# Performance work log

Hardware: AMD Instinct MI355X
Metric: run time of the kernel (lower is better)

The kernel has to match this reference:

```python
import jax, jax.numpy as jnp
import numpy as np

B, T, D, U = 64, 512, 512, 1024


def setup_inputs() -> dict:
    key = jax.random.key(0)
    k1, k2, k3 = jax.random.split(key, 3)
    x = jax.random.normal(k1, (B, T, D), dtype=jnp.float32)
    kernel = jax.random.normal(k2, (D, 4 * U), dtype=jnp.float32) * (1.0 / np.sqrt(D))
    rec_kernel = jax.random.normal(k3, (U, 4 * U), dtype=jnp.float32) * (1.0 / np.sqrt(U))
    return {"x": x, "kernel": kernel, "rec_kernel": rec_kernel}


def reference(x, kernel, rec_kernel):
    """SimpleLSTM forward: returns last hidden state h_T of shape [B, U].
    Gate order along the 4U axis is (i, f, c, o), matching the kernel split.
    No biases; initial h and c are zeros (as in the original call()).
    """
    units = rec_kernel.shape[0]
    # Precompute input contributions for all timesteps in one big GEMM:
    # x_gates[b, t, :] == x[b, t] @ kernel  (same math as 4 per-gate matmuls)
    x_gates = jnp.einsum('btd,dk->tbk', x, kernel)  # [T, B, 4U]

    def step(carry, xt):
        h, c = carry
        z = xt + h @ rec_kernel  # [B, 4U]
        i = jax.nn.sigmoid(z[:, :units])
        f = jax.nn.sigmoid(z[:, units:2 * units])
        g = jnp.tanh(z[:, 2 * units:3 * units])
        o = jax.nn.sigmoid(z[:, 3 * units:])
        c_new = f * c + i * g
        h_new = o * jnp.tanh(c_new)
        return (h_new, c_new), None

    batch = x.shape[0]
    h0 = jnp.zeros((batch, units), dtype=x.dtype)
    c0 = jnp.zeros((batch, units), dtype=x.dtype)
    (h_last, _), _ = jax.lax.scan(step, (h0, c0), x_gates)
    return h_last
```

## Files before the change

### kernel.cpp

```cpp
#include <hip/hip_runtime.h>
#include <stdint.h>

#define WS_XB   0LL
#define WS_H    33554432LL
#define WS_FLAG 33816576LL

typedef unsigned short u16;
typedef unsigned int   u32;
typedef unsigned long long u64;
typedef __attribute__((ext_vector_type(8))) short short8;
typedef __attribute__((ext_vector_type(4))) float f32x4;

__device__ __forceinline__ u16 f2bf(float f) {
  unsigned u = __float_as_uint(f);
  u += 0x7FFFu + ((u >> 16) & 1u);
  return (u16)(u >> 16);
}
__device__ __forceinline__ float fast_tanh(float x) {
  float e = __expf(2.f * x);
  return 1.f - 2.f / (e + 1.f);
}

__global__ void conv_x(const float* __restrict__ x, u16* __restrict__ xb) {
  long gid = (long)blockIdx.x * blockDim.x + threadIdx.x;
  long sr = gid >> 6;
  int  d0 = (int)(gid & 63) * 8;
  int  b = (int)(sr >> 9), t = (int)(sr & 511);
  const float* src = x + sr * 512 + d0;
  float4 v0 = *(const float4*)(src);
  float4 v1 = *(const float4*)(src + 4);
  u16 tmp[8] = {f2bf(v0.x), f2bf(v0.y), f2bf(v0.z), f2bf(v0.w),
                f2bf(v1.x), f2bf(v1.y), f2bf(v1.z), f2bf(v1.w)};
  *(short8*)(xb + ((long)t * 64 + b) * 512 + d0) = *(short8*)tmp;
}

__launch_bounds__(256, 1)
__global__ void lstm_fused(const float* __restrict__ kern, const float* __restrict__ rec,
                           const u16* __restrict__ xb, u32* __restrict__ hbuf,
                           u32* __restrict__ flags, float* __restrict__ out) {
  __shared__ u16   smH[32 * 64 * 8];
  __shared__ float zbuf[4 * 16 * 17];

  const int bid = blockIdx.x;
  const int bg = bid >> 6;
  const int ut = bid & 63;
  const int tid = threadIdx.x;
  const int w = tid >> 6, lane = tid & 63;
  const int quad = lane >> 4, n15 = lane & 15;

  short8 wf[48];
  const size_t gcol = (size_t)w * 1024 + (size_t)ut * 16 + (size_t)n15;
#pragma unroll
  for (int ks = 0; ks < 32; ++ks) {
    u16 tmp[8];
#pragma unroll
    for (int j = 0; j < 8; ++j)
      tmp[j] = f2bf(rec[(size_t)(ks * 32 + quad * 8 + j) * 4096 + gcol]);
    wf[ks] = *(short8*)tmp;
  }
#pragma unroll
  for (int ks = 0; ks < 16; ++ks) {
    u16 tmp[8];
#pragma unroll
    for (int j = 0; j < 8; ++j)
      tmp[j] = f2bf(kern[(size_t)(ks * 32 + quad * 8 + j) * 4096 + gcol]);
    wf[32 + ks] = *(short8*)tmp;
  }

  const int bl = tid >> 4;
  const int ul = tid & 15;
  float c = 0.f;

#pragma unroll
  for (int j = 0; j < 8; ++j)
    *(uint4*)(smH + (tid + j * 256) * 8) = (uint4){0u, 0u, 0u, 0u};

  short8 xf[16];
  {
    const u16* xr = xb + (size_t)(bg * 16 + n15) * 512 + quad * 8;
#pragma unroll
    for (int ks = 0; ks < 16; ++ks) xf[ks] = *(const short8*)(xr + ks * 32);
  }
  __syncthreads();

  for (int t = 0; t < 512; ++t) {
    f32x4 acc0 = {0.f, 0.f, 0.f, 0.f}, acc1 = {0.f, 0.f, 0.f, 0.f};
#pragma unroll
    for (int ks = 0; ks < 32; ks += 2) {
      short8 a0 = *(const short8*)(smH + (ks * 64 + lane) * 8);
      acc0 = __builtin_amdgcn_mfma_f32_16x16x32_bf16(a0, wf[ks], acc0, 0, 0, 0);
      short8 a1 = *(const short8*)(smH + ((ks + 1) * 64 + lane) * 8);
      acc1 = __builtin_amdgcn_mfma_f32_16x16x32_bf16(a1, wf[ks + 1], acc1, 0, 0, 0);
    }
#pragma unroll
    for (int ks = 0; ks < 16; ks += 2) {
      acc0 = __builtin_amdgcn_mfma_f32_16x16x32_bf16(xf[ks], wf[32 + ks], acc0, 0, 0, 0);
      acc1 = __builtin_amdgcn_mfma_f32_16x16x32_bf16(xf[ks + 1], wf[33 + ks], acc1, 0, 0, 0);
    }

    float* zp = zbuf + (w * 16 + quad * 4) * 17 + n15;
    zp[0]  = acc0[0] + acc1[0];
    zp[17] = acc0[1] + acc1[1];
    zp[34] = acc0[2] + acc1[2];
    zp[51] = acc0[3] + acc1[3];
    __syncthreads();

    float zi = zbuf[(0 * 16 + bl) * 17 + ul];
    float zf = zbuf[(1 * 16 + bl) * 17 + ul];
    float zg = zbuf[(2 * 16 + bl) * 17 + ul];
    float zo = zbuf[(3 * 16 + bl) * 17 + ul];
    float ig = 1.f / (1.f + __expf(-zi));
    float fg = 1.f / (1.f + __expf(-zf));
    float gg = fast_tanh(zg);
    float og = 1.f / (1.f + __expf(-zo));
    c = fg * c + ig * gg;
    float h = og * fast_tanh(c);

    if (t == 511) {
      out[(size_t)(bg * 16 + bl) * 1024 + (size_t)ut * 16 + ul] = h;
      break;
    }

    const int pb = (t + 1) & 1;

    {
      u16 hu = f2bf(h);
      int other = __shfl_xor((int)(unsigned)hu, 1);
      if ((tid & 1) == 0) {
        u32 v = (u32)hu | ((u32)(unsigned)other << 16);
        __hip_atomic_store(&hbuf[(size_t)pb * 32768 + (size_t)(bg * 16 + bl) * 512
                                 + ut * 8 + (ul >> 1)],
                           v, __ATOMIC_RELAXED, __HIP_MEMORY_SCOPE_AGENT);
      }
    }
    __builtin_amdgcn_s_waitcnt(0x0F70);
    __syncthreads();

    if (tid == 0)
      __hip_atomic_store(&flags[(bg * 64 + ut) * 32], (u32)(t + 1),
                         __ATOMIC_RELAXED, __HIP_MEMORY_SCOPE_AGENT);

    if (w != 0) {
      const u16* xr = xb + ((size_t)(t + 1) * 64 + bg * 16 + n15) * 512 + quad * 8;
#pragma unroll
      for (int ks = 0; ks < 16; ++ks) xf[ks] = *(const short8*)(xr + ks * 32);
    }

    if (w == 0) {
      const u32 tgt = (u32)(t + 1);
      const u32* fp = &flags[(bg * 64 + lane) * 32];
      u32 v = __hip_atomic_load(fp, __ATOMIC_RELAXED, __HIP_MEMORY_SCOPE_AGENT);
      while (__ballot(v < tgt) != 0ull) {
        __builtin_amdgcn_s_sleep(1);
        v = __hip_atomic_load(fp, __ATOMIC_RELAXED, __HIP_MEMORY_SCOPE_AGENT);
      }
    }
    __syncthreads();

    if (w == 0) {
      const u16* xr = xb + ((size_t)(t + 1) * 64 + bg * 16 + n15) * 512 + quad * 8;
#pragma unroll
      for (int ks = 0; ks < 16; ++ks) xf[ks] = *(const short8*)(xr + ks * 32);
    }

    {
      const u32* hs = hbuf + (size_t)pb * 32768 + (size_t)(bg * 16 + n15) * 512;
#pragma unroll
      for (int kk = 0; kk < 8; ++kk) {
        const int ks = w * 8 + kk;
        const u64* src = (const u64*)(hs + ks * 16 + quad * 4);
        u64 v0 = __hip_atomic_load(src,     __ATOMIC_RELAXED, __HIP_MEMORY_SCOPE_AGENT);
        u64 v1 = __hip_atomic_load(src + 1, __ATOMIC_RELAXED, __HIP_MEMORY_SCOPE_AGENT);
        u64 pair[2] = {v0, v1};
        *(uint4*)(smH + (ks * 64 + lane) * 8) = *(const uint4*)pair;
      }
    }
    __syncthreads();
  }
}

extern "C" void kernel_launch(void* const* d_in, const int* in_sizes, int n_in,
                              void* d_out, int out_size, void* d_ws, size_t ws_size,
                              hipStream_t stream) {
  const float* x    = (const float*)d_in[0];
  const float* kern = (const float*)d_in[1];
  const float* rec  = (const float*)d_in[2];
  float* out = (float*)d_out;
  char* ws = (char*)d_ws;

  u16* xbp   = (u16*)(ws + WS_XB);
  u32* hbuf  = (u32*)(ws + WS_H);
  u32* flags = (u32*)(ws + WS_FLAG);

  hipMemsetAsync(ws + WS_FLAG, 0, 32768, stream);

  conv_x<<<8192, 256, 0, stream>>>(x, xbp);

  lstm_fused<<<256, 256, 0, stream>>>(kern, rec, xbp, hbuf, flags, out);
}
```

Before: 3.425 ms.

## Replace per-block flag barrier with tagged hidden-state words polled directly

Each hidden value is now stored as a 32-bit word with the bf16 value in the high half and the timestep tag in the low half. Consumers spin on the h data itself until every tag matches, so the separate flag store, waitcnt, extra block barriers and flag-polling wave are removed. The intended saving is inter-block handshake latency on every recurrent step. In exchange the hbuf traffic doubles, and every wave now polls global memory instead of a single wave.

After: 3.944 ms. 15.1% more time.

```diff
diff --git a/kernel.cpp b/kernel.cpp
--- a/kernel.cpp
+++ b/kernel.cpp
@@ -3,7 +3,6 @@
 
 #define WS_XB   0LL
 #define WS_H    33554432LL
-#define WS_FLAG 33816576LL
 
 typedef unsigned short u16;
 typedef unsigned int   u32;
@@ -37,7 +36,7 @@
 __launch_bounds__(256, 1)
 __global__ void lstm_fused(const float* __restrict__ kern, const float* __restrict__ rec,
                            const u16* __restrict__ xb, u32* __restrict__ hbuf,
-                           u32* __restrict__ flags, float* __restrict__ out) {
+                           float* __restrict__ out) {
   __shared__ u16   smH[32 * 64 * 8];
   __shared__ float zbuf[4 * 16 * 17];
 
@@ -122,57 +121,49 @@
     }
 
     const int pb = (t + 1) & 1;
+    const u32 tag = (u32)(t + 1);
+
+    __hip_atomic_store(&hbuf[(size_t)pb * 65536 + (size_t)(bg * 16 + bl) * 1024
+                             + ut * 16 + ul],
+                       ((u32)f2bf(h) << 16) | tag,
+                       __ATOMIC_RELAXED, __HIP_MEMORY_SCOPE_AGENT);
 
     {
-      u16 hu = f2bf(h);
-      int other = __shfl_xor((int)(unsigned)hu, 1);
-      if ((tid & 1) == 0) {
-        u32 v = (u32)hu | ((u32)(unsigned)other << 16);
-        __hip_atomic_store(&hbuf[(size_t)pb * 32768 + (size_t)(bg * 16 + bl) * 512
-                                 + ut * 8 + (ul >> 1)],
-                           v, __ATOMIC_RELAXED, __HIP_MEMORY_SCOPE_AGENT);
-      }
-    }
-    __builtin_amdgcn_s_waitcnt(0x0F70);
-    __syncthreads();
-
-    if (tid == 0)
-      __hip_atomic_store(&flags[(bg * 64 + ut) * 32], (u32)(t + 1),
-                         __ATOMIC_RELAXED, __HIP_MEMORY_SCOPE_AGENT);
-
-    if (w != 0) {
-      const u16* xr = xb + ((size_t)(t + 1) * 64 + bg * 16 + n15) * 512 + quad * 8;
-#pragma unroll
-      for (int ks = 0; ks < 16; ++ks) xf[ks] = *(const short8*)(xr + ks * 32);
-    }
-
-    if (w == 0) {
-      const u32 tgt = (u32)(t + 1);
-      const u32* fp = &flags[(bg * 64 + lane) * 32];
-      u32 v = __hip_atomic_load(fp, __ATOMIC_RELAXED, __HIP_MEMORY_SCOPE_AGENT);
-      while (__ballot(v < tgt) != 0ull) {
-        __builtin_amdgcn_s_sleep(1);
-        v = __hip_atomic_load(fp, __ATOMIC_RELAXED, __HIP_MEMORY_SCOPE_AGENT);
-      }
-    }
-    __syncthreads();
-
-    if (w == 0) {
       const u16* xr = xb + ((size_t)(t + 1) * 64 + bg * 16 + n15) * 512 + quad * 8;
 #pragma unroll
       for (int ks = 0; ks < 16; ++ks) xf[ks] = *(const short8*)(xr + ks * 32);
     }
 
     {
-      const u32* hs = hbuf + (size_t)pb * 32768 + (size_t)(bg * 16 + n15) * 512;
+      const u32* hb = hbuf + (size_t)pb * 65536 + (size_t)(bg * 16 + n15) * 1024;
+      const u32 tagtag = tag | (tag << 16);
+      u64 v[32];
+      for (;;) {
+#pragma unroll
+        for (int kk = 0; kk < 8; ++kk) {
+          const u64* src = (const u64*)(hb + (w * 8 + kk) * 32 + quad * 8);
+          v[kk * 4 + 0] = __hip_atomic_load(src + 0, __ATOMIC_RELAXED, __HIP_MEMORY_SCOPE_AGENT);
+          v[kk * 4 + 1] = __hip_atomic_load(src + 1, __ATOMIC_RELAXED, __HIP_MEMORY_SCOPE_AGENT);
+          v[kk * 4 + 2] = __hip_atomic_load(src + 2, __ATOMIC_RELAXED, __HIP_MEMORY_SCOPE_AGENT);
+          v[kk * 4 + 3] = __hip_atomic_load(src + 3, __ATOMIC_RELAXED, __HIP_MEMORY_SCOPE_AGENT);
+        }
+        u32 diff = 0;
+#pragma unroll
+        for (int i = 0; i < 32; ++i) {
+          u32 lo = (u32)v[i], hi = (u32)(v[i] >> 32);
+          diff |= (__builtin_amdgcn_perm(hi, lo, 0x05040100u) ^ tagtag);
+        }
+        if (diff == 0) break;
+      }
 #pragma unroll
       for (int kk = 0; kk < 8; ++kk) {
-        const int ks = w * 8 + kk;
-        const u64* src = (const u64*)(hs + ks * 16 + quad * 4);
-        u64 v0 = __hip_atomic_load(src,     __ATOMIC_RELAXED, __HIP_MEMORY_SCOPE_AGENT);
-        u64 v1 = __hip_atomic_load(src + 1, __ATOMIC_RELAXED, __HIP_MEMORY_SCOPE_AGENT);
-        u64 pair[2] = {v0, v1};
-        *(uint4*)(smH + (ks * 64 + lane) * 8) = *(const uint4*)pair;
+        u32 o[4];
+#pragma unroll
+        for (int p = 0; p < 4; ++p) {
+          u32 lo = (u32)v[kk * 4 + p], hi = (u32)(v[kk * 4 + p] >> 32);
+          o[p] = __builtin_amdgcn_perm(hi, lo, 0x07060302u);
+        }
+        *(uint4*)(smH + ((w * 8 + kk) * 64 + lane) * 8) = *(uint4*)o;
       }
     }
     __syncthreads();
@@ -188,13 +179,12 @@
   float* out = (float*)d_out;
   char* ws = (char*)d_ws;
 
-  u16* xbp   = (u16*)(ws + WS_XB);
-  u32* hbuf  = (u32*)(ws + WS_H);
-  u32* flags = (u32*)(ws + WS_FLAG);
+  u16* xbp  = (u16*)(ws + WS_XB);
+  u32* hbuf = (u32*)(ws + WS_H);
 
-  hipMemsetAsync(ws + WS_FLAG, 0, 32768, stream);
+  hipMemsetAsync(ws + WS_H, 0, 524288, stream);
 
   conv_x<<<8192, 256, 0, stream>>>(x, xbp);
 
-  lstm_fused<<<256, 256, 0, stream>>>(kern, rec, xbp, hbuf, flags, out);
+  lstm_fused<<<256, 256, 0, stream>>>(kern, rec, xbp, hbuf, out);
 }
```
